# Kernel tuning notes

Hardware: AMD Instinct MI355X
Metric: run time of the kernel (lower is better)

The kernel has to match this reference:

```python
import jax, jax.numpy as jnp
import numpy as np

N_NODES = 100000
N_EDGES = 1600000
IN_DIM = 128
OUT_DIM = 128
ORDER = 2
EPS = 1e-9


def setup_inputs() -> dict:
    key = jax.random.key(0)
    ks = jax.random.split(key, 4)
    features = jax.random.normal(ks[0], (N_NODES, IN_DIM), dtype=jnp.float32)
    src = jax.random.randint(ks[1], (N_EDGES,), 0, N_NODES)
    dst = jax.random.randint(ks[2], (N_EDGES,), 0, N_NODES)
    w = jnp.ones((N_EDGES,), dtype=jnp.float32)
    D_norm = jax.random.uniform(ks[3], (N_NODES, 1), dtype=jnp.float32)
    # xavier-normal-ish init for the order+1 linear weights
    Wk = jax.random.split(jax.random.key(1), ORDER + 1)
    std = np.sqrt(2.0 / (IN_DIM + OUT_DIM)).astype(np.float32)
    W = jnp.stack([jax.random.normal(k, (OUT_DIM, IN_DIM), dtype=jnp.float32) * std for k in Wk])
    b = jnp.zeros((ORDER + 1, OUT_DIM), dtype=jnp.float32)
    scale = jnp.ones((ORDER + 1, OUT_DIM), dtype=jnp.float32)
    offset = jnp.zeros((ORDER + 1, OUT_DIM), dtype=jnp.float32)
    return {"features": features, "src": src, "dst": dst, "w": w,
            "D_norm": D_norm, "W": W, "b": b, "scale": scale, "offset": offset}


def reference(features, src, dst, w, D_norm, W, b, scale, offset):
    N = features.shape[0]

    def feat_trans(ft, i):
        h = ft @ W[i].T + b[i]          # [N, out]
        h = jax.nn.relu(h)
        mean = jnp.mean(h, axis=1, keepdims=True)
        var = jnp.var(h, axis=1, keepdims=True) + EPS  # unbiased=False
        return (h - mean) * scale[i] * jax.lax.rsqrt(var) + offset[i]

    h_hop = [features]
    for _ in range(ORDER):
        m = h_hop[-1][src] * w[:, None]                 # u_mul_e gather  [E, d]
        agg = jax.ops.segment_sum(m, dst, num_segments=N)  # sum reduce to dst
        h_hop.append(agg * D_norm)

    h_part = [feat_trans(ft, i) for i, ft in enumerate(h_hop)]
    return jnp.concatenate(h_part, axis=1)  # aggr='concat' -> [N, (order+1)*out]
```

## Files before the change

### kernel.cpp

```cpp
#include <hip/hip_runtime.h>
#include <hip/hip_bf16.h>

#define OUT_STRIDE 384
#define EPSV 1e-9f
#define BSH 10
#define BS 1024
#define NBMAX 512
#define CH 4096

typedef __attribute__((ext_vector_type(8))) short bf16x8;
typedef __attribute__((ext_vector_type(4))) float f32x4;

static __device__ __forceinline__ unsigned short f2bf(float f) {
    __hip_bfloat16 h = __float2bfloat16(f);
    return *reinterpret_cast<unsigned short*>(&h);
}

__global__ __launch_bounds__(256)
void bhist_kernel(const int* __restrict__ dst, int* __restrict__ bcnt, int E, int NB) {
    __shared__ int h[NBMAX];
    for (int i = threadIdx.x; i < NBMAX; i += 256) h[i] = 0;
    __syncthreads();
    int i = blockIdx.x * blockDim.x + threadIdx.x;
    int stride = gridDim.x * blockDim.x;
    for (; i < E; i += stride) atomicAdd(&h[dst[i] >> BSH], 1);
    __syncthreads();
    for (int j = threadIdx.x; j < NB; j += 256)
        if (h[j]) atomicAdd(&bcnt[j], h[j]);
}

__global__ __launch_bounds__(256)
void bscan_kernel(const int* __restrict__ bcnt, int* __restrict__ bbase,
                  int* __restrict__ bcur, int* __restrict__ off,
                  int NB, int N, int E) {
    const int t = threadIdx.x;
    const int lane = t & 63, wv = t >> 6;
    int b0 = 2 * t, b1 = 2 * t + 1;
    int c0 = (b0 < NB) ? bcnt[b0] : 0;
    int c1 = (b1 < NB) ? bcnt[b1] : 0;
    int s = c0 + c1;
    int inc = s;
    #pragma unroll
    for (int d = 1; d < 64; d <<= 1) { int u = __shfl_up(inc, d); if (lane >= d) inc += u; }
    __shared__ int wt[4];
    if (lane == 63) wt[wv] = inc;
    __syncthreads();
    int base = 0;
    for (int w2 = 0; w2 < wv; ++w2) base += wt[w2];
    int ex = base + inc - s;
    if (b0 < NB) { bbase[b0] = ex;      bcur[b0] = ex; }
    if (b1 < NB) { bbase[b1] = ex + c0; bcur[b1] = ex + c0; }
    if (t == 0) { bbase[NB] = E; off[N] = E; }
}

__global__ __launch_bounds__(256)
void multisplit_kernel(const int* __restrict__ src, const int* __restrict__ dst,
                       const float* __restrict__ w, int* __restrict__ bcur,
                       int* __restrict__ rec, int E) {
    __shared__ int hist[NBMAX], scan_[NBMAX], gbase[NBMAX], lcur[NBMAX];
    __shared__ int recS[CH * 3];
    __shared__ int wt[4];
    const int t = threadIdx.x;
    const int lane = t & 63, wv = t >> 6;
    const int c0 = blockIdx.x * CH;
    const int cnt_total = min(CH, E - c0);

    for (int i = t; i < NBMAX; i += 256) hist[i] = 0;
    __syncthreads();
    #pragma unroll
    for (int p = 0; p < CH / 256; ++p) {
        int i = c0 + p * 256 + t;
        if (i < E) atomicAdd(&hist[dst[i] >> BSH], 1);
    }
    __syncthreads();
    {
        int b0 = 2 * t, b1 = 2 * t + 1;
        int h0 = hist[b0], h1 = hist[b1];
        int s = h0 + h1;
        int inc = s;
        #pragma unroll
        for (int d = 1; d < 64; d <<= 1) { int u = __shfl_up(inc, d); if (lane >= d) inc += u; }
        if (lane == 63) wt[wv] = inc;
        __syncthreads();
        int base = 0;
        for (int w2 = 0; w2 < wv; ++w2) base += wt[w2];
        int ex = base + inc - s;
        scan_[b0] = ex;
        scan_[b1] = ex + h0;
    }
    __syncthreads();
    for (int i = t; i < NBMAX; i += 256) {
        if (hist[i] > 0) gbase[i] = atomicAdd(&bcur[i], hist[i]);
        lcur[i] = scan_[i];
    }
    __syncthreads();
    #pragma unroll
    for (int p = 0; p < CH / 256; ++p) {
        int i = c0 + p * 256 + t;
        if (i < E) {
            int d = dst[i];
            int b = d >> BSH;
            int j = atomicAdd(&lcur[b], 1);
            recS[3 * j]     = src[i];
            recS[3 * j + 1] = d;
            recS[3 * j + 2] = __float_as_int(w[i]);
        }
    }
    __syncthreads();
    #pragma unroll
    for (int p = 0; p < CH / 256; ++p) {
        int j = p * 256 + t;
        if (j < cnt_total) {
            int d = recS[3 * j + 1];
            int b = d >> BSH;
            int g = gbase[b] + (j - scan_[b]);
            rec[3 * g]     = recS[3 * j];
            rec[3 * g + 1] = d;
            rec[3 * g + 2] = recS[3 * j + 2];
        }
    }
}

__global__ __launch_bounds__(256)
void bucket_csr_kernel(const int* __restrict__ rec, const int* __restrict__ bbase,
                       int* __restrict__ off, int2* __restrict__ ed, int N) {
    __shared__ int h[BS];
    __shared__ int wt[4];
    const int b = blockIdx.x;
    const int t = threadIdx.x;
    const int lane = t & 63, wv = t >> 6;
    const int e0 = bbase[b], e1 = bbase[b + 1];
    const int n0 = b << BSH;
    const int nn = min(BS, N - n0);

    for (int i = t; i < BS; i += 256) h[i] = 0;
    __syncthreads();
    for (int i = e0 + t; i < e1; i += 256) atomicAdd(&h[rec[3 * i + 1] - n0], 1);
    __syncthreads();
    {
        int j0 = 4 * t;
        int l0 = h[j0], l1 = h[j0 + 1], l2 = h[j0 + 2], l3 = h[j0 + 3];
        int s = l0 + l1 + l2 + l3;
        int inc = s;
        #pragma unroll
        for (int d = 1; d < 64; d <<= 1) { int u = __shfl_up(inc, d); if (lane >= d) inc += u; }
        if (lane == 63) wt[wv] = inc;
        __syncthreads();
        int base = 0;
        for (int w2 = 0; w2 < wv; ++w2) base += wt[w2];
        int ex = base + inc - s;
        int e_[4] = {ex, ex + l0, ex + l0 + l1, ex + l0 + l1 + l2};
        __syncthreads();
        #pragma unroll
        for (int k = 0; k < 4; ++k) {
            h[j0 + k] = e_[k];
            if (j0 + k < nn) off[n0 + j0 + k] = e0 + e_[k];
        }
    }
    __syncthreads();
    for (int i = e0 + t; i < e1; i += 256) {
        int d = rec[3 * i + 1] - n0;
        int pos = atomicAdd(&h[d], 1);
        ed[e0 + pos] = make_int2(rec[3 * i], rec[3 * i + 2]);
    }
}

__global__ __launch_bounds__(256)
void pack_kernel(const float* __restrict__ in, unsigned short* __restrict__ outb, long n4) {
    long i = blockIdx.x * blockDim.x + threadIdx.x;
    long stride = (long)gridDim.x * blockDim.x;
    for (; i < n4; i += stride) {
        float4 v = ((const float4*)in)[i];
        ushort4 o;
        o.x = f2bf(v.x); o.y = f2bf(v.y); o.z = f2bf(v.z); o.w = f2bf(v.w);
        *(ushort4*)&outb[i * 4] = o;
    }
}

__device__ __forceinline__ void acc8(float* a, int4 r, float w) {
    #pragma unroll
    for (int j = 0; j < 4; ++j) {
        int bits = (&r.x)[j];
        float f0 = __int_as_float(bits << 16);
        float f1 = __int_as_float(bits & 0xffff0000);
        a[2 * j]     += f0 * w;
        a[2 * j + 1] += f1 * w;
    }
}

__global__ __launch_bounds__(256)
void gather_bf16in(const unsigned short* __restrict__ X,
                   const int* __restrict__ off, const int2* __restrict__ ed,
                   const float* __restrict__ Dn,
                   unsigned short* __restrict__ outb,
                   float* __restrict__ outf, long ocol0, int N) {
    const int tid = threadIdx.x;
    const int l = tid & 15;
    const int n = blockIdx.x * 16 + (tid >> 4);
    if (n >= N) return;
    const int beg = off[n], end = off[n + 1];
    float a[8] = {0.f, 0.f, 0.f, 0.f, 0.f, 0.f, 0.f, 0.f};
    const unsigned short* Xc = X + 8 * l;
    int i = beg;
    for (; i + 3 < end; i += 4) {
        int2 e0 = ed[i], e1 = ed[i + 1], e2 = ed[i + 2], e3 = ed[i + 3];
        int4 r0 = *(const int4*)(Xc + (long)e0.x * 128);
        int4 r1 = *(const int4*)(Xc + (long)e1.x * 128);
        int4 r2 = *(const int4*)(Xc + (long)e2.x * 128);
        int4 r3 = *(const int4*)(Xc + (long)e3.x * 128);
        acc8(a, r0, __int_as_float(e0.y));
        acc8(a, r1, __int_as_float(e1.y));
        acc8(a, r2, __int_as_float(e2.y));
        acc8(a, r3, __int_as_float(e3.y));
    }
    for (; i < end; ++i) {
        int2 e0 = ed[i];
        int4 r0 = *(const int4*)(Xc + (long)e0.x * 128);
        acc8(a, r0, __int_as_float(e0.y));
    }
    const float dn = Dn[n];
    #pragma unroll
    for (int j = 0; j < 8; ++j) a[j] *= dn;
    if (outb) {
        int4 o;
        #pragma unroll
        for (int j = 0; j < 4; ++j) {
            unsigned lo = f2bf(a[2 * j]);
            unsigned hi = f2bf(a[2 * j + 1]);
            (&o.x)[j] = (int)((hi << 16) | lo);
        }
        *(int4*)&outb[(long)n * 128 + 8 * l] = o;
    } else {
        float* p = outf + (long)n * OUT_STRIDE + ocol0 + 8 * l;
        *(float4*)p       = make_float4(a[0], a[1], a[2], a[3]);
        *(float4*)(p + 4) = make_float4(a[4], a[5], a[6], a[7]);
    }
}

__global__ __launch_bounds__(256)
void scatter_kernel(const float* X, long xstride, long xcol0,
                    const int* __restrict__ src, const int* __restrict__ dst,
                    const float* __restrict__ w, const float* __restrict__ Dn,
                    int useDn, float* out, long ocol0, int nE)
{
    const int lane = threadIdx.x & 63;
    const int wave = (int)((blockIdx.x * blockDim.x + threadIdx.x) >> 6);
    const int nWaves = (int)((gridDim.x * blockDim.x) >> 6);
    for (int e = wave; e < nE; e += nWaves) {
        const int s = src[e];
        const int d = dst[e];
        float ww = w[e];
        if (useDn) ww *= Dn[s];
        const float2 v = *(const float2*)(X + (long)s * xstride + xcol0 + 2 * lane);
        float* o = out + (long)d * OUT_STRIDE + ocol0 + 2 * lane;
        atomicAdd(o, v.x * ww);
        atomicAdd(o + 1, v.y * ww);
    }
}

__global__ __launch_bounds__(256)
void transform_kernel(const void* x0, int f0, long s0,
                      const void* x1, int f1, long s1,
                      const void* x2, int f2, long s2,
                      const float* __restrict__ Dn,
                      const float* __restrict__ Wf,
                      const float* __restrict__ bf,
                      const float* __restrict__ scf,
                      const float* __restrict__ off,
                      float* out, int N, int applyDn)
{
    const int hop = blockIdx.y;
    const int tid = threadIdx.x;
    const int lane = tid & 63;
    const int wv = tid >> 6;

    constexpr int XS = 136;
    __shared__ __attribute__((aligned(16))) short Wl[128 * XS];
    __shared__ __attribute__((aligned(16))) short Xl[64 * XS];

    const float4* W4 = (const float4*)(Wf + (long)hop * 128 * 128);
    for (int idx = tid; idx < 128 * 32; idx += 256) {
        float4 v = W4[idx];
        int row = idx >> 5;
        int col = (idx & 31) * 4;
        short* p = &Wl[row * XS + col];
        p[0] = f2bf(v.x); p[1] = f2bf(v.y); p[2] = f2bf(v.z); p[3] = f2bf(v.w);
    }
    const void* xp = (hop == 0) ? x0 : (hop == 1) ? x1 : x2;
    const int fmt  = (hop == 0) ? f0 : (hop == 1) ? f1 : f2;
    const long xs  = (hop == 0) ? s0 : (hop == 1) ? s1 : s2;
    const int n0 = blockIdx.x * 64;
    if (fmt) {
        const unsigned short* xb = (const unsigned short*)xp;
        for (int idx = tid; idx < 64 * 16; idx += 256) {
            int r = idx >> 4;
            int c = (idx & 15) * 8;
            int n = n0 + r;
            int4 v = make_int4(0, 0, 0, 0);
            if (n < N) v = *(const int4*)(xb + (long)n * xs + c);
            *(int4*)&Xl[r * XS + c] = v;
        }
    } else {
        const float* xf = (const float*)xp;
        for (int idx = tid; idx < 64 * 32; idx += 256) {
            int r = idx >> 5;
            int col = (idx & 31) * 4;
            int n = n0 + r;
            float4 v = make_float4(0.f, 0.f, 0.f, 0.f);
            float m = 1.0f;
            if (n < N) {
                v = *(const float4*)(xf + (long)n * xs + col);
                if (applyDn && hop > 0) m = Dn[n];
            }
            short* p = &Xl[r * XS + col];
            p[0] = f2bf(v.x * m); p[1] = f2bf(v.y * m); p[2] = f2bf(v.z * m); p[3] = f2bf(v.w * m);
        }
    }
    __syncthreads();

    f32x4 acc[8];
    #pragma unroll
    for (int c = 0; c < 8; ++c) acc[c] = (f32x4){0.f, 0.f, 0.f, 0.f};
    const int rsub = lane & 15;
    const int g = lane >> 4;
    const short* xbase = &Xl[(wv * 16 + rsub) * XS + g * 8];
    const short* wbase = &Wl[rsub * XS + g * 8];
    #pragma unroll
    for (int kk = 0; kk < 4; ++kk) {
        bf16x8 a = *(const bf16x8*)(xbase + kk * 32);
        #pragma unroll
        for (int c = 0; c < 8; ++c) {
            bf16x8 bb = *(const bf16x8*)(wbase + c * 16 * XS + kk * 32);
            acc[c] = __builtin_amdgcn_mfma_f32_16x16x32_bf16(a, bb, acc[c], 0, 0, 0);
        }
    }

    const float* bp = bf  + hop * 128;
    const float* sp = scf + hop * 128;
    const float* op = off + hop * 128;
    float sum[4] = {0.f, 0.f, 0.f, 0.f};
    float ssq[4] = {0.f, 0.f, 0.f, 0.f};
    #pragma unroll
    for (int c = 0; c < 8; ++c) {
        float bias = bp[c * 16 + rsub];
        #pragma unroll
        for (int r = 0; r < 4; ++r) {
            float h = acc[c][r] + bias;
            h = fmaxf(h, 0.0f);
            acc[c][r] = h;
            sum[r] += h;
            ssq[r] += h * h;
        }
    }
    #pragma unroll
    for (int msk = 1; msk < 16; msk <<= 1) {
        #pragma unroll
        for (int r = 0; r < 4; ++r) {
            sum[r] += __shfl_xor(sum[r], msk);
            ssq[r] += __shfl_xor(ssq[r], msk);
        }
    }
    #pragma unroll
    for (int r = 0; r < 4; ++r) {
        int n = n0 + wv * 16 + g * 4 + r;
        if (n >= N) continue;
        float mean = sum[r] * (1.0f / 128.0f);
        float var = ssq[r] * (1.0f / 128.0f) - mean * mean + EPSV;
        float inv = rsqrtf(var);
        float* orow = out + (long)n * OUT_STRIDE + hop * 128;
        #pragma unroll
        for (int c = 0; c < 8; ++c) {
            int col = c * 16 + rsub;
            orow[col] = (acc[c][r] - mean) * sp[col] * inv + op[col];
        }
    }
}

extern "C" void kernel_launch(void* const* d_in, const int* in_sizes, int n_in,
                              void* d_out, int out_size, void* d_ws, size_t ws_size,
                              hipStream_t stream) {
    const float* features = (const float*)d_in[0];
    const int*   src      = (const int*)d_in[1];
    const int*   dst      = (const int*)d_in[2];
    const float* w        = (const float*)d_in[3];
    const float* Dn       = (const float*)d_in[4];
    const float* W        = (const float*)d_in[5];
    const float* b        = (const float*)d_in[6];
    const float* scale    = (const float*)d_in[7];
    const float* offset   = (const float*)d_in[8];
    float* out = (float*)d_out;
    const int N = in_sizes[0] / 128;
    const int E = in_sizes[1];
    const int NB = (N + BS - 1) >> BSH;

    const size_t o_off = 0;
    const size_t o_ed  = ((size_t)N + 1 + 3) & ~(size_t)3;
    const size_t o_b   = o_ed + 2 * (size_t)E;
    const size_t o_uni = (o_b + 3 * (size_t)NB + 1 + 3) & ~(size_t)3;
    const size_t uni2  = (size_t)128 * N > 3 * (size_t)E ? (size_t)128 * N : 3 * (size_t)E;
    const size_t uni3  = (size_t)192 * N > 3 * (size_t)E ? (size_t)192 * N : 3 * (size_t)E;
    const size_t need2 = (o_uni + uni2) * 4;
    const size_t need3 = (o_uni + uni3) * 4;
    dim3 tg((N + 63) / 64, 3);

    if (NB <= NBMAX && ws_size >= need2) {
        int* ws_i  = (int*)d_ws;
        int* off   = ws_i + o_off;
        int2* ed   = (int2*)(ws_i + o_ed);
        int* bcnt  = ws_i + o_b;
        int* bbase = bcnt + NB;
        int* bcur  = bbase + NB + 1;
        int* rec   = ws_i + o_uni;
        unsigned short* featb = (unsigned short*)(ws_i + o_uni);
        unsigned short* h1b   = featb + (size_t)N * 128;
        unsigned short* h2b   = h1b + (size_t)N * 128;
        const int use_h2b = (ws_size >= need3);

        hipMemsetAsync(bcnt, 0, (size_t)NB * 4, stream);
        bhist_kernel<<<512, 256, 0, stream>>>(dst, bcnt, E, NB);
        bscan_kernel<<<1, 256, 0, stream>>>(bcnt, bbase, bcur, off, NB, N, E);
        multisplit_kernel<<<(E + CH - 1) / CH, 256, 0, stream>>>(src, dst, w, bcur, rec, E);
        bucket_csr_kernel<<<NB, 256, 0, stream>>>(rec, bbase, off, ed, N);

        pack_kernel<<<2048, 256, 0, stream>>>(features, featb, (long)N * 32);
        gather_bf16in<<<(N + 15) / 16, 256, 0, stream>>>(featb, off, ed, Dn, h1b, nullptr, 0, N);
        if (use_h2b) {
            gather_bf16in<<<(N + 15) / 16, 256, 0, stream>>>(h1b, off, ed, Dn, h2b, nullptr, 0, N);
            transform_kernel<<<tg, 256, 0, stream>>>(
                featb, 1, 128, h1b, 1, 128, h2b, 1, 128,
                Dn, W, b, scale, offset, out, N, 0);
        } else {
            gather_bf16in<<<(N + 15) / 16, 256, 0, stream>>>(h1b, off, ed, Dn, nullptr, out, 256, N);
            transform_kernel<<<tg, 256, 0, stream>>>(
                featb, 1, 128, h1b, 1, 128, out + 256, 0, OUT_STRIDE,
                Dn, W, b, scale, offset, out, N, 0);
        }
    } else {
        hipMemsetAsync(out, 0, (size_t)out_size * sizeof(float), stream);
        scatter_kernel<<<2048, 256, 0, stream>>>(features, 128, 0, src, dst, w, Dn, 0, out, 128, E);
        scatter_kernel<<<2048, 256, 0, stream>>>(out, OUT_STRIDE, 128, src, dst, w, Dn, 1, out, 256, E);
        transform_kernel<<<tg, 256, 0, stream>>>(
            features, 0, 128, out + 128, 0, OUT_STRIDE, out + 256, 0, OUT_STRIDE,
            Dn, W, b, scale, offset, out, N, 1);
    }
}
```

Before: 360.2 us.

## Fuse feature transform and layer norm into pack and gather kernels

Merges the per-hop linear+ReLU+layernorm transform into the kernels that produce each hop: the bf16 pack kernel does hop 0, and each gather kernel aggregates 64 nodes into shared memory and then runs the MFMA epilogue. This removes the separate transform kernel, the h2 bf16 buffer, and the re-reads of the hop features from global memory. In exchange each gather block must restage W into LDS, and each thread handles 4 nodes in sequence, which may cut gather parallelism and occupancy. The multisplit chunk size is also halved.

Result: slower. 402.1 us (+11.6%).

```diff
diff --git a/kernel.cpp b/kernel.cpp
--- a/kernel.cpp
+++ b/kernel.cpp
@@ -6,7 +6,7 @@
 #define BSH 10
 #define BS 1024
 #define NBMAX 512
-#define CH 4096
+#define CH 2048
 
 typedef __attribute__((ext_vector_type(8))) short bf16x8;
 typedef __attribute__((ext_vector_type(4))) float f32x4;
@@ -165,16 +165,107 @@
     }
 }
 
-__global__ __launch_bounds__(256)
-void pack_kernel(const float* __restrict__ in, unsigned short* __restrict__ outb, long n4) {
-    long i = blockIdx.x * blockDim.x + threadIdx.x;
-    long stride = (long)gridDim.x * blockDim.x;
-    for (; i < n4; i += stride) {
-        float4 v = ((const float4*)in)[i];
-        ushort4 o;
-        o.x = f2bf(v.x); o.y = f2bf(v.y); o.z = f2bf(v.z); o.w = f2bf(v.w);
-        *(ushort4*)&outb[i * 4] = o;
-    }
+#define XS 136
+
+__device__ __forceinline__ void stage_W(const float* __restrict__ Wf_hop, short* Wl, int tid) {
+    const float4* W4 = (const float4*)Wf_hop;
+    for (int idx = tid; idx < 128 * 32; idx += 256) {
+        float4 v = W4[idx];
+        int row = idx >> 5;
+        int col = (idx & 31) * 4;
+        short* p = &Wl[row * XS + col];
+        p[0] = f2bf(v.x); p[1] = f2bf(v.y); p[2] = f2bf(v.z); p[3] = f2bf(v.w);
+    }
+}
+
+__device__ __forceinline__ void mfma_ln_epilogue(
+    const short* Xl, const short* Wl,
+    const float* __restrict__ bp, const float* __restrict__ sp, const float* __restrict__ op,
+    float* out, int ocol, int n0, int N, int tid)
+{
+    const int lane = tid & 63;
+    const int wv = tid >> 6;
+    f32x4 acc[8];
+    #pragma unroll
+    for (int c = 0; c < 8; ++c) acc[c] = (f32x4){0.f, 0.f, 0.f, 0.f};
+    const int rsub = lane & 15;
+    const int g = lane >> 4;
+    const short* xbase = &Xl[(wv * 16 + rsub) * XS + g * 8];
+    const short* wbase = &Wl[rsub * XS + g * 8];
+    #pragma unroll
+    for (int kk = 0; kk < 4; ++kk) {
+        bf16x8 a = *(const bf16x8*)(xbase + kk * 32);
+        #pragma unroll
+        for (int c = 0; c < 8; ++c) {
+            bf16x8 bb = *(const bf16x8*)(wbase + c * 16 * XS + kk * 32);
+            acc[c] = __builtin_amdgcn_mfma_f32_16x16x32_bf16(a, bb, acc[c], 0, 0, 0);
+        }
+    }
+    float sum[4] = {0.f, 0.f, 0.f, 0.f};
+    float ssq[4] = {0.f, 0.f, 0.f, 0.f};
+    #pragma unroll
+    for (int c = 0; c < 8; ++c) {
+        float bias = bp[c * 16 + rsub];
+        #pragma unroll
+        for (int r = 0; r < 4; ++r) {
+            float h = acc[c][r] + bias;
+            h = fmaxf(h, 0.0f);
+            acc[c][r] = h;
+            sum[r] += h;
+            ssq[r] += h * h;
+        }
+    }
+    #pragma unroll
+    for (int msk = 1; msk < 16; msk <<= 1) {
+        #pragma unroll
+        for (int r = 0; r < 4; ++r) {
+            sum[r] += __shfl_xor(sum[r], msk);
+            ssq[r] += __shfl_xor(ssq[r], msk);
+        }
+    }
+    #pragma unroll
+    for (int r = 0; r < 4; ++r) {
+        int n = n0 + wv * 16 + g * 4 + r;
+        if (n >= N) continue;
+        float mean = sum[r] * (1.0f / 128.0f);
+        float var = ssq[r] * (1.0f / 128.0f) - mean * mean + EPSV;
+        float inv = rsqrtf(var);
+        float* orow = out + (long)n * OUT_STRIDE + ocol;
+        #pragma unroll
+        for (int c = 0; c < 8; ++c) {
+            int col = c * 16 + rsub;
+            orow[col] = (acc[c][r] - mean) * sp[col] * inv + op[col];
+        }
+    }
+}
+
+__global__ __launch_bounds__(256)
+void packT_kernel(const float* __restrict__ features,
+                  const float* __restrict__ Wf,
+                  const float* __restrict__ bf, const float* __restrict__ scf,
+                  const float* __restrict__ offp,
+                  unsigned short* __restrict__ featb,
+                  float* __restrict__ out, int N)
+{
+    __shared__ __attribute__((aligned(16))) short Wl[128 * XS];
+    __shared__ __attribute__((aligned(16))) short Xl[64 * XS];
+    const int tid = threadIdx.x;
+    stage_W(Wf, Wl, tid);
+    const int n0 = blockIdx.x * 64;
+    for (int idx = tid; idx < 64 * 32; idx += 256) {
+        int r = idx >> 5;
+        int col = (idx & 31) * 4;
+        int n = n0 + r;
+        ushort4 o = make_ushort4(0, 0, 0, 0);
+        if (n < N) {
+            float4 v = *(const float4*)(features + (long)n * 128 + col);
+            o.x = f2bf(v.x); o.y = f2bf(v.y); o.z = f2bf(v.z); o.w = f2bf(v.w);
+            *(ushort4*)&featb[(long)n * 128 + col] = o;
+        }
+        *(ushort4*)&Xl[r * XS + col] = o;
+    }
+    __syncthreads();
+    mfma_ln_epilogue(Xl, Wl, bf, scf, offp, out, 0, n0, N, tid);
 }
 
 __device__ __forceinline__ void acc8(float* a, int4 r, float w) {
@@ -189,52 +280,65 @@
 }
 
 __global__ __launch_bounds__(256)
-void gather_bf16in(const unsigned short* __restrict__ X,
-                   const int* __restrict__ off, const int2* __restrict__ ed,
-                   const float* __restrict__ Dn,
-                   unsigned short* __restrict__ outb,
-                   float* __restrict__ outf, long ocol0, int N) {
+void gatherT_kernel(const unsigned short* __restrict__ X,
+                    const int* __restrict__ off, const int2* __restrict__ ed,
+                    const float* __restrict__ Dn,
+                    const float* __restrict__ Wf_hop,
+                    const float* __restrict__ bp, const float* __restrict__ sp,
+                    const float* __restrict__ op,
+                    unsigned short* __restrict__ rowout,
+                    float* __restrict__ out, int ocol, int N)
+{
+    __shared__ __attribute__((aligned(16))) short Wl[128 * XS];
+    __shared__ __attribute__((aligned(16))) short Xl[64 * XS];
     const int tid = threadIdx.x;
+    stage_W(Wf_hop, Wl, tid);
+
     const int l = tid & 15;
-    const int n = blockIdx.x * 16 + (tid >> 4);
-    if (n >= N) return;
-    const int beg = off[n], end = off[n + 1];
-    float a[8] = {0.f, 0.f, 0.f, 0.f, 0.f, 0.f, 0.f, 0.f};
+    const int grp = tid >> 4;
+    const int n0 = blockIdx.x * 64;
     const unsigned short* Xc = X + 8 * l;
-    int i = beg;
-    for (; i + 3 < end; i += 4) {
-        int2 e0 = ed[i], e1 = ed[i + 1], e2 = ed[i + 2], e3 = ed[i + 3];
-        int4 r0 = *(const int4*)(Xc + (long)e0.x * 128);
-        int4 r1 = *(const int4*)(Xc + (long)e1.x * 128);
-        int4 r2 = *(const int4*)(Xc + (long)e2.x * 128);
-        int4 r3 = *(const int4*)(Xc + (long)e3.x * 128);
-        acc8(a, r0, __int_as_float(e0.y));
-        acc8(a, r1, __int_as_float(e1.y));
-        acc8(a, r2, __int_as_float(e2.y));
-        acc8(a, r3, __int_as_float(e3.y));
-    }
-    for (; i < end; ++i) {
-        int2 e0 = ed[i];
-        int4 r0 = *(const int4*)(Xc + (long)e0.x * 128);
-        acc8(a, r0, __int_as_float(e0.y));
-    }
-    const float dn = Dn[n];
-    #pragma unroll
-    for (int j = 0; j < 8; ++j) a[j] *= dn;
-    if (outb) {
-        int4 o;
-        #pragma unroll
-        for (int j = 0; j < 4; ++j) {
-            unsigned lo = f2bf(a[2 * j]);
-            unsigned hi = f2bf(a[2 * j + 1]);
-            (&o.x)[j] = (int)((hi << 16) | lo);
-        }
-        *(int4*)&outb[(long)n * 128 + 8 * l] = o;
-    } else {
-        float* p = outf + (long)n * OUT_STRIDE + ocol0 + 8 * l;
-        *(float4*)p       = make_float4(a[0], a[1], a[2], a[3]);
-        *(float4*)(p + 4) = make_float4(a[4], a[5], a[6], a[7]);
-    }
+    #pragma unroll
+    for (int q = 0; q < 4; ++q) {
+        int n = n0 + grp * 4 + q;
+        int r = grp * 4 + q;
+        if (n < N) {
+            const int beg = off[n], end = off[n + 1];
+            float a[8] = {0.f, 0.f, 0.f, 0.f, 0.f, 0.f, 0.f, 0.f};
+            int i = beg;
+            for (; i + 3 < end; i += 4) {
+                int2 e0 = ed[i], e1 = ed[i + 1], e2 = ed[i + 2], e3 = ed[i + 3];
+                int4 r0 = *(const int4*)(Xc + (long)e0.x * 128);
+                int4 r1 = *(const int4*)(Xc + (long)e1.x * 128);
+                int4 r2 = *(const int4*)(Xc + (long)e2.x * 128);
+                int4 r3 = *(const int4*)(Xc + (long)e3.x * 128);
+                acc8(a, r0, __int_as_float(e0.y));
+                acc8(a, r1, __int_as_float(e1.y));
+                acc8(a, r2, __int_as_float(e2.y));
+                acc8(a, r3, __int_as_float(e3.y));
+            }
+            for (; i < end; ++i) {
+                int2 e0 = ed[i];
+                int4 r0 = *(const int4*)(Xc + (long)e0.x * 128);
+                acc8(a, r0, __int_as_float(e0.y));
+            }
+            const float dn = Dn[n];
+            int4 o;
+            #pragma unroll
+            for (int j = 0; j < 4; ++j) {
+                unsigned lo = f2bf(a[2 * j] * dn);
+                unsigned hi = f2bf(a[2 * j + 1] * dn);
+                (&o.x)[j] = (int)((hi << 16) | lo);
+            }
+            *(int4*)&Xl[r * XS + 8 * l] = o;
+            if (rowout) *(int4*)&rowout[(long)n * 128 + 8 * l] = o;
+        } else {
+            int4 z = make_int4(0, 0, 0, 0);
+            *(int4*)&Xl[r * XS + 8 * l] = z;
+        }
+    }
+    __syncthreads();
+    mfma_ln_epilogue(Xl, Wl, bp, sp, op, out, ocol, n0, N, tid);
 }
 
 __global__ __launch_bounds__(256)
@@ -259,121 +363,33 @@
 }
 
 __global__ __launch_bounds__(256)
-void transform_kernel(const void* x0, int f0, long s0,
-                      const void* x1, int f1, long s1,
-                      const void* x2, int f2, long s2,
-                      const float* __restrict__ Dn,
-                      const float* __restrict__ Wf,
-                      const float* __restrict__ bf,
-                      const float* __restrict__ scf,
-                      const float* __restrict__ off,
-                      float* out, int N, int applyDn)
+void transform_f32_kernel(const float* x, long xs, int useDnIn,
+                          const float* __restrict__ Dn,
+                          const float* __restrict__ Wf_hop,
+                          const float* __restrict__ bp, const float* __restrict__ sp,
+                          const float* __restrict__ op,
+                          float* out, int ocol, int N)
 {
-    const int hop = blockIdx.y;
-    const int tid = threadIdx.x;
-    const int lane = tid & 63;
-    const int wv = tid >> 6;
-
-    constexpr int XS = 136;
     __shared__ __attribute__((aligned(16))) short Wl[128 * XS];
     __shared__ __attribute__((aligned(16))) short Xl[64 * XS];
-
-    const float4* W4 = (const float4*)(Wf + (long)hop * 128 * 128);
-    for (int idx = tid; idx < 128 * 32; idx += 256) {
-        float4 v = W4[idx];
-        int row = idx >> 5;
+    const int tid = threadIdx.x;
+    stage_W(Wf_hop, Wl, tid);
+    const int n0 = blockIdx.x * 64;
+    for (int idx = tid; idx < 64 * 32; idx += 256) {
+        int r = idx >> 5;
         int col = (idx & 31) * 4;
-        short* p = &Wl[row * XS + col];
-        p[0] = f2bf(v.x); p[1] = f2bf(v.y); p[2] = f2bf(v.z); p[3] = f2bf(v.w);
-    }
-    const void* xp = (hop == 0) ? x0 : (hop == 1) ? x1 : x2;
-    const int fmt  = (hop == 0) ? f0 : (hop == 1) ? f1 : f2;
-    const long xs  = (hop == 0) ? s0 : (hop == 1) ? s1 : s2;
-    const int n0 = blockIdx.x * 64;
-    if (fmt) {
-        const unsigned short* xb = (const unsigned short*)xp;
-        for (int idx = tid; idx < 64 * 16; idx += 256) {
-            int r = idx >> 4;
-            int c = (idx & 15) * 8;
-            int n = n0 + r;
-            int4 v = make_int4(0, 0, 0, 0);
-            if (n < N) v = *(const int4*)(xb + (long)n * xs + c);
-            *(int4*)&Xl[r * XS + c] = v;
-        }
-    } else {
-        const float* xf = (const float*)xp;
-        for (int idx = tid; idx < 64 * 32; idx += 256) {
-            int r = idx >> 5;
-            int col = (idx & 31) * 4;
-            int n = n0 + r;
-            float4 v = make_float4(0.f, 0.f, 0.f, 0.f);
-            float m = 1.0f;
-            if (n < N) {
-                v = *(const float4*)(xf + (long)n * xs + col);
-                if (applyDn && hop > 0) m = Dn[n];
-            }
-            short* p = &Xl[r * XS + col];
-            p[0] = f2bf(v.x * m); p[1] = f2bf(v.y * m); p[2] = f2bf(v.z * m); p[3] = f2bf(v.w * m);
-        }
-    }
-    __syncthreads();
-
-    f32x4 acc[8];
-    #pragma unroll
-    for (int c = 0; c < 8; ++c) acc[c] = (f32x4){0.f, 0.f, 0.f, 0.f};
-    const int rsub = lane & 15;
-    const int g = lane >> 4;
-    const short* xbase = &Xl[(wv * 16 + rsub) * XS + g * 8];
-    const short* wbase = &Wl[rsub * XS + g * 8];
-    #pragma unroll
-    for (int kk = 0; kk < 4; ++kk) {
-        bf16x8 a = *(const bf16x8*)(xbase + kk * 32);
-        #pragma unroll
-        for (int c = 0; c < 8; ++c) {
-            bf16x8 bb = *(const bf16x8*)(wbase + c * 16 * XS + kk * 32);
-            acc[c] = __builtin_amdgcn_mfma_f32_16x16x32_bf16(a, bb, acc[c], 0, 0, 0);
-        }
-    }
-
-    const float* bp = bf  + hop * 128;
-    const float* sp = scf + hop * 128;
-    const float* op = off + hop * 128;
-    float sum[4] = {0.f, 0.f, 0.f, 0.f};
-    float ssq[4] = {0.f, 0.f, 0.f, 0.f};
-    #pragma unroll
-    for (int c = 0; c < 8; ++c) {
-        float bias = bp[c * 16 + rsub];
-        #pragma unroll
-        for (int r = 0; r < 4; ++r) {
-            float h = acc[c][r] + bias;
-            h = fmaxf(h, 0.0f);
-            acc[c][r] = h;
-            sum[r] += h;
-            ssq[r] += h * h;
-        }
-    }
-    #pragma unroll
-    for (int msk = 1; msk < 16; msk <<= 1) {
-        #pragma unroll
-        for (int r = 0; r < 4; ++r) {
-            sum[r] += __shfl_xor(sum[r], msk);
-            ssq[r] += __shfl_xor(ssq[r], msk);
-        }
-    }
-    #pragma unroll
-    for (int r = 0; r < 4; ++r) {
-        int n = n0 + wv * 16 + g * 4 + r;
-        if (n >= N) continue;
-        float mean = sum[r] * (1.0f / 128.0f);
-        float var = ssq[r] * (1.0f / 128.0f) - mean * mean + EPSV;
-        float inv = rsqrtf(var);
-        float* orow = out + (long)n * OUT_STRIDE + hop * 128;
-        #pragma unroll
-        for (int c = 0; c < 8; ++c) {
-            int col = c * 16 + rsub;
-            orow[col] = (acc[c][r] - mean) * sp[col] * inv + op[col];
-        }
-    }
+        int n = n0 + r;
+        float4 v = make_float4(0.f, 0.f, 0.f, 0.f);
+        float m = 1.0f;
+        if (n < N) {
+            v = *(const float4*)(x + (long)n * xs + col);
+            if (useDnIn) m = Dn[n];
+        }
+        short* p = &Xl[r * XS + col];
+        p[0] = f2bf(v.x * m); p[1] = f2bf(v.y * m); p[2] = f2bf(v.z * m); p[3] = f2bf(v.w * m);
+    }
+    __syncthreads();
+    mfma_ln_epilogue(Xl, Wl, bp, sp, op, out, ocol, n0, N, tid);
 }
 
 extern "C" void kernel_launch(void* const* d_in, const int* in_sizes, int n_in,
@@ -397,13 +413,11 @@
     const size_t o_ed  = ((size_t)N + 1 + 3) & ~(size_t)3;
     const size_t o_b   = o_ed + 2 * (size_t)E;
     const size_t o_uni = (o_b + 3 * (size_t)NB + 1 + 3) & ~(size_t)3;
-    const size_t uni2  = (size_t)128 * N > 3 * (size_t)E ? (size_t)128 * N : 3 * (size_t)E;
-    const size_t uni3  = (size_t)192 * N > 3 * (size_t)E ? (size_t)192 * N : 3 * (size_t)E;
-    const size_t need2 = (o_uni + uni2) * 4;
-    const size_t need3 = (o_uni + uni3) * 4;
-    dim3 tg((N + 63) / 64, 3);
-
-    if (NB <= NBMAX && ws_size >= need2) {
+    const size_t uni   = (size_t)128 * N > 3 * (size_t)E ? (size_t)128 * N : 3 * (size_t)E;
+    const size_t need  = (o_uni + uni) * 4;
+    const int nblk = (N + 63) / 64;
+
+    if (NB <= NBMAX && ws_size >= need) {
         int* ws_i  = (int*)d_ws;
         int* off   = ws_i + o_off;
         int2* ed   = (int2*)(ws_i + o_ed);
@@ -413,8 +427,6 @@
         int* rec   = ws_i + o_uni;
         unsigned short* featb = (unsigned short*)(ws_i + o_uni);
         unsigned short* h1b   = featb + (size_t)N * 128;
-        unsigned short* h2b   = h1b + (size_t)N * 128;
-        const int use_h2b = (ws_size >= need3);
 
         hipMemsetAsync(bcnt, 0, (size_t)NB * 4, stream);
         bhist_kernel<<<512, 256, 0, stream>>>(dst, bcnt, E, NB);
@@ -422,25 +434,17 @@
         multisplit_kernel<<<(E + CH - 1) / CH, 256, 0, stream>>>(src, dst, w, bcur, rec, E);
         bucket_csr_kernel<<<NB, 256, 0, stream>>>(rec, bbase, off, ed, N);
 
-        pack_kernel<<<2048, 256, 0, stream>>>(features, featb, (long)N * 32);
-        gather_bf16in<<<(N + 15) / 16, 256, 0, stream>>>(featb, off, ed, Dn, h1b, nullptr, 0, N);
-        if (use_h2b) {
-            gather_bf16in<<<(N + 15) / 16, 256, 0, stream>>>(h1b, off, ed, Dn, h2b, nullptr, 0, N);
-            transform_kernel<<<tg, 256, 0, stream>>>(
-                featb, 1, 128, h1b, 1, 128, h2b, 1, 128,
-                Dn, W, b, scale, offset, out, N, 0);
-        } else {
-            gather_bf16in<<<(N + 15) / 16, 256, 0, stream>>>(h1b, off, ed, Dn, nullptr, out, 256, N);
-            transform_kernel<<<tg, 256, 0, stream>>>(
-                featb, 1, 128, h1b, 1, 128, out + 256, 0, OUT_STRIDE,
-                Dn, W, b, scale, offset, out, N, 0);
-        }
+        packT_kernel<<<nblk, 256, 0, stream>>>(features, W, b, scale, offset, featb, out, N);
+        gatherT_kernel<<<nblk, 256, 0, stream>>>(featb, off, ed, Dn,
+                W + 128 * 128, b + 128, scale + 128, offset + 128, h1b, out, 128, N);
+        gatherT_kernel<<<nblk, 256, 0, stream>>>(h1b, off, ed, Dn,
+                W + 2 * 128 * 128, b + 256, scale + 256, offset + 256, nullptr, out, 256, N);
     } else {
         hipMemsetAsync(out, 0, (size_t)out_size * sizeof(float), stream);
         scatter_kernel<<<2048, 256, 0, stream>>>(features, 128, 0, src, dst, w, Dn, 0, out, 128, E);
         scatter_kernel<<<2048, 256, 0, stream>>>(out, OUT_STRIDE, 128, src, dst, w, Dn, 1, out, 256, E);
-        transform_kernel<<<tg, 256, 0, stream>>>(
-            features, 0, 128, out + 128, 0, OUT_STRIDE, out + 256, 0, OUT_STRIDE,
-            Dn, W, b, scale, offset, out, N, 1);
-    }
-}
+        transform_f32_kernel<<<nblk, 256, 0, stream>>>(features, 128, 0, Dn, W, b, scale, offset, out, 0, N);
+        transform_f32_kernel<<<nblk, 256, 0, stream>>>(out + 128, OUT_STRIDE, 1, Dn, W + 128 * 128, b + 128, scale + 128, offset + 128, out, 128, N);
+        transform_f32_kernel<<<nblk, 256, 0, stream>>>(out + 256, OUT_STRIDE, 1, Dn, W + 2 * 128 * 128, b + 256, scale + 256, offset + 256, out, 256, N);
+    }
+}
```
